# Performance work log

Measured on AMD Instinct MI355X. Metric: run time of the kernel, lower is better.

Reference implementation:

```python
import jax, jax.numpy as jnp
import numpy as np

LN_EPS = 1e-5

def silu(x):
    return x * jax.nn.sigmoid(x)

def setup_inputs() -> dict:
    key = jax.random.key(0)
    ks = jax.random.split(key, 24)
    B, D = 131072, 256
    def w(k, shape, fan_in):
        return jax.random.uniform(k, shape, jnp.float32, -1.0, 1.0) / np.sqrt(fan_in)
    inp = {
        'x': jax.random.normal(ks[0], (B, D), jnp.float32),
        # stem: Linear(D,128) -> LN(128) -> SiLU -> Linear(128,64) -> SiLU
        'stem_w1': w(ks[1], (D, 128), D), 'stem_b1': w(ks[2], (128,), D),
        'ln_g': jnp.ones((128,), jnp.float32), 'ln_b': jnp.zeros((128,), jnp.float32),
        'stem_w2': w(ks[3], (128, 64), 128), 'stem_b2': w(ks[4], (64,), 128),
        # 4 experts: Linear(64,128)->SiLU->Linear(128,64)->SiLU, stacked on axis 0
        'ew1': w(ks[5], (4, 64, 128), 64), 'eb1': w(ks[6], (4, 128), 64),
        'ew2': w(ks[7], (4, 128, 64), 128), 'eb2': w(ks[8], (4, 64), 128),
        # gate: Linear(64,32)->SiLU->Linear(32,4)
        'gw1': w(ks[9], (64, 32), 64), 'gb1': w(ks[10], (32,), 64),
        'gw2': w(ks[11], (32, 4), 32), 'gb2': w(ks[12], (4,), 32),
        # shared: Linear(64,64)->SiLU
        'sw': w(ks[13], (64, 64), 64), 'sb': w(ks[14], (64,), 64),
        # 3 heads (strain, tensile, yield) stacked: Linear(64,32)->SiLU->Linear(32,1)
        'hw1': w(ks[15], (3, 64, 32), 64), 'hb1': w(ks[16], (3, 32), 64),
        'hw2': w(ks[17], (3, 32, 1), 32), 'hb2': w(ks[18], (3, 1), 32),
    }
    return inp

def reference(x, stem_w1, stem_b1, ln_g, ln_b, stem_w2, stem_b2,
              ew1, eb1, ew2, eb2, gw1, gb1, gw2, gb2, sw, sb,
              hw1, hb1, hw2, hb2):
    # stem (dropout = identity, eval mode)
    h = x @ stem_w1 + stem_b1                      # [B,128]
    mu = jnp.mean(h, -1, keepdims=True)
    var = jnp.mean(jnp.square(h - mu), -1, keepdims=True)
    h = (h - mu) * jax.lax.rsqrt(var + LN_EPS) * ln_g + ln_b
    h = silu(h)
    h = silu(h @ stem_w2 + stem_b2)                # [B,64]
    # gate
    g = silu(h @ gw1 + gb1)
    gate_w = jax.nn.softmax(g @ gw2 + gb2, axis=-1)  # [B,4]
    # experts: [B,64] x [4,64,128] -> [B,4,128]
    e = silu(jnp.einsum('bd,edh->beh', h, ew1) + eb1)
    e = silu(jnp.einsum('beh,ehd->bed', e, ew2) + eb2)  # [B,4,64]
    moe_h = jnp.einsum('bed,be->bd', e, gate_w)    # [B,64]
    # shared trunk (dropout = identity)
    feat = silu(moe_h @ sw + sb)                   # [B,64]
    # 3 heads
    hh = silu(jnp.einsum('bd,kdh->bkh', feat, hw1) + hb1)  # [B,3,32]
    out = (jnp.einsum('bkh,kho->bko', hh, hw2) + hb2)[..., 0]  # [B,3]
    return out
```

## Files before the change

### kernel.cpp

```cpp
#include <hip/hip_runtime.h>

typedef _Float16 f16;
typedef f16   f16x4 __attribute__((ext_vector_type(4)));
typedef f16   f16x8 __attribute__((ext_vector_type(8)));
typedef float f32x4 __attribute__((ext_vector_type(4)));
typedef __attribute__((address_space(3))) char as3char;

#define MFMA16(a, b, c) __builtin_amdgcn_mfma_f32_16x16x32_f16((a), (b), (c), 0, 0, 0)

#define IMG_W1   0
#define IMG_W2   32768
#define IMG_GW1  40960
#define IMG_E    43008
#define IMG_SWH  108544
#define IMG_HW2G 116736

__device__ __forceinline__ float silu_f(float v) {
    return v * __builtin_amdgcn_rcpf(1.0f + __expf(-v));
}

__device__ void conv_blk(const float* __restrict__ src, f16* __restrict__ dst,
                         int srcN, int k0, int n0, int KB, int NB, int tid, int nth) {
    for (int i = tid; i < KB * NB; i += nth) {
        const int kk = i / NB, nn = i - kk * NB;
        dst[nn * KB + (kk ^ ((nn & 7) << 3))] = (f16)src[(long)(k0 + kk) * srcN + n0 + nn];
    }
}

__global__ void prep_weights(const float* __restrict__ w1, const float* __restrict__ w2,
                             const float* __restrict__ gw1, const float* __restrict__ ew1,
                             const float* __restrict__ ew2, const float* __restrict__ sw,
                             const float* __restrict__ hw1, f16* __restrict__ ws) {
    const int tid = blockIdx.x * 256 + threadIdx.x;
    const int nth = gridDim.x * 256;
    for (int kq = 0; kq < 4; ++kq)
        for (int nh = 0; nh < 2; ++nh)
            conv_blk(w1, ws + IMG_W1 + (kq * 2 + nh) * 4096, 128, kq * 64, nh * 64, 64, 64, tid, nth);
    for (int kh = 0; kh < 2; ++kh)
        conv_blk(w2, ws + IMG_W2 + kh * 4096, 64, kh * 64, 0, 64, 64, tid, nth);
    conv_blk(gw1, ws + IMG_GW1, 32, 0, 0, 64, 32, tid, nth);
    for (int e = 0; e < 4; ++e)
        for (int h = 0; h < 2; ++h) {
            conv_blk(ew1 + e * 8192, ws + IMG_E + e * 16384 + h * 8192,        128, 0, h * 64, 64, 64, tid, nth);
            conv_blk(ew2 + e * 8192, ws + IMG_E + e * 16384 + h * 8192 + 4096,  64, h * 64, 0, 64, 64, tid, nth);
        }
    conv_blk(sw, ws + IMG_SWH, 64, 0, 0, 64, 64, tid, nth);
    for (int h = 0; h < 2; ++h)
        conv_blk(hw1 + h * 2048, ws + IMG_SWH + 4096 + h * 2048, 32, 0, 0, 64, 32, tid, nth);
    conv_blk(hw1 + 2 * 2048, ws + IMG_HW2G, 32, 0, 0, 64, 32, tid, nth);
}

template<int BYTES>
__device__ __forceinline__ void stage4(const f16* __restrict__ g, as3char* l, int wv, int lane) {
    constexpr int CH = BYTES / 1024;
    #pragma unroll
    for (int ch = 0; ch < CH; ++ch)
        if ((ch & 3) == wv)
            __builtin_amdgcn_global_load_lds(
                (const __attribute__((address_space(1))) void*)((const char*)g + ch * 1024 + lane * 16),
                (__attribute__((address_space(3))) void*)(l + ch * 1024), 16, 0, 0);
}

__device__ __forceinline__ int swzW(int n) { return (n & 7) << 3; }
__device__ __forceinline__ int swzS(int r) { return (((((r >> 2) & 3) << 1) | (r & 1))) << 3; }

__device__ __forceinline__ f16x8 ldW(const f16* base, int row_base, int k0, int lane) {
    const int r = row_base + (lane & 15);
    const int k = k0 + ((lane >> 4) << 3);
    return *(const f16x8*)(base + r * 64 + (k ^ swzW(r)));
}
__device__ __forceinline__ f16x8 ldS(const f16* strip, int k0, int lane) {
    const int r = lane & 15;
    const int k = k0 + ((lane >> 4) << 3);
    return *(const f16x8*)(strip + r * 64 + (k ^ swzS(r)));
}
__device__ __forceinline__ void stS(f16* strip, int col_base, f32x4 v, int lane) {
    const int cc = col_base + (lane & 15);
    #pragma unroll
    for (int g = 0; g < 4; ++g) {
        const int r = ((lane >> 4) << 2) + g;
        strip[r * 64 + (cc ^ swzS(r))] = (f16)v[g];
    }
}

__device__ __forceinline__ void mm8(const f16x8 a[2], const f16* wb, f32x4 acc[4], int lane) {
    #pragma unroll
    for (int ks = 0; ks < 2; ++ks)
        #pragma unroll
        for (int n = 0; n < 4; ++n) {
            const f16x8 b = ldW(wb, n * 16, ks * 32, lane);
            acc[n] = MFMA16(a[ks], b, acc[n]);
        }
}

__device__ __forceinline__ void silu_to_frags(f16* strip, const f32x4 in[4], f16x8 outf[2], int lane) {
    #pragma unroll
    for (int n = 0; n < 4; ++n) {
        f32x4 v;
        #pragma unroll
        for (int g = 0; g < 4; ++g) v[g] = silu_f(in[n][g]);
        stS(strip, n * 16, v, lane);
    }
    #pragma unroll
    for (int ks = 0; ks < 2; ++ks)
        outf[ks] = ldS(strip, ks * 32, lane);
}

__device__ __forceinline__ f32x4 reduce16(f32x4 v) {
    #pragma unroll
    for (int m = 1; m <= 8; m <<= 1) {
        f32x4 o;
        #pragma unroll
        for (int i = 0; i < 4; ++i) o[i] = __shfl_xor(v[i], m, 64);
        v += o;
    }
    return v;
}

__global__ __launch_bounds__(256, 5)
void fused_net_mfma(const float* __restrict__ x,   const f16* __restrict__ wsp,
                    const float* __restrict__ b1,  const float* __restrict__ lng,
                    const float* __restrict__ lnb, const float* __restrict__ b2,
                    const float* __restrict__ eb1, const float* __restrict__ eb2,
                    const float* __restrict__ gb1, const float* __restrict__ gw2,
                    const float* __restrict__ gb2, const float* __restrict__ sb,
                    const float* __restrict__ hb1, const float* __restrict__ hw2,
                    const float* __restrict__ hb2, float* __restrict__ out)
{
    __shared__ __align__(16) f16 lds[14592];
    as3char* const LB = (as3char*)lds;
    const int lane = threadIdx.x & 63;
    const int wv   = threadIdx.x >> 6;
    const int c    = lane & 15;
    const int q    = lane >> 4;
    f16* STRIP = lds + wv * 1024;
    f16* const WB0 = lds + 4096;   as3char* const WB_3 = LB + 8192;
    f16* const WB1 = lds + 8192;
    f16* const G   = lds + 12288;  as3char* const G_3  = LB + 24576;
    f16* const GWT = lds + 14336;

    const long blockRow = (long)blockIdx.x * 64;
    const float* xw = x + (blockRow + wv * 16) * 256;

    stage4<16384>(wsp + IMG_W1, WB_3, wv, lane);
    stage4<4096>(wsp + IMG_GW1, G_3, wv, lane);
    __syncthreads();

    f32x4 acc[8];
    #pragma unroll
    for (int n8 = 0; n8 < 8; ++n8) {
        const float bv = b1[n8 * 16 + c];
        f32x4 t = {bv, bv, bv, bv};
        acc[n8] = t;
    }

    #pragma unroll 1
    for (int kq = 0; kq < 4; ++kq) {
        #pragma unroll
        for (int i = 0; i < 4; ++i) {
            const int idx4 = lane + i * 64;
            const int r  = idx4 >> 4;
            const int c4 = (idx4 & 15) << 2;
            const float4 v = *(const float4*)(xw + r * 256 + kq * 64 + c4);
            f16x4 o; o[0] = (f16)v.x; o[1] = (f16)v.y; o[2] = (f16)v.z; o[3] = (f16)v.w;
            *(f16x4*)(STRIP + r * 64 + (c4 ^ swzS(r))) = o;
        }
        f16x8 af[2];
        #pragma unroll
        for (int ks = 0; ks < 2; ++ks)
            af[ks] = ldS(STRIP, ks * 32, lane);

        mm8(af, WB0, acc,     lane);
        mm8(af, WB1, acc + 4, lane);
        __syncthreads();
        const f16* nsrc = (kq < 3) ? (wsp + IMG_W1 + (kq + 1) * 8192) : (wsp + IMG_W2);
        stage4<16384>(nsrc, WB_3, wv, lane);
        __syncthreads();
    }

    f32x4 mu, rs;
    {
        f32x4 s = {0,0,0,0}, qq = {0,0,0,0};
        #pragma unroll
        for (int n8 = 0; n8 < 8; ++n8) { s += acc[n8]; qq += acc[n8] * acc[n8]; }
        s = reduce16(s); qq = reduce16(qq);
        mu = s * 0.0078125f;
        #pragma unroll
        for (int g = 0; g < 4; ++g)
            rs[g] = rsqrtf(qq[g] * 0.0078125f - mu[g] * mu[g] + 1e-5f);
    }

    f32x4 a2[4];
    #pragma unroll
    for (int n = 0; n < 4; ++n) {
        const float bv = b2[n * 16 + c];
        f32x4 t = {bv, bv, bv, bv};
        a2[n] = t;
    }
    #pragma unroll
    for (int kh = 0; kh < 2; ++kh) {
        #pragma unroll
        for (int n = 0; n < 4; ++n) {
            const int j = kh * 64 + n * 16 + c;
            const float gg = lng[j], bb = lnb[j];
            f32x4 v;
            #pragma unroll
            for (int g = 0; g < 4; ++g)
                v[g] = silu_f((acc[kh * 4 + n][g] - mu[g]) * rs[g] * gg + bb);
            stS(STRIP, n * 16, v, lane);
        }
        f16x8 af[2];
        #pragma unroll
        for (int ks = 0; ks < 2; ++ks)
            af[ks] = ldS(STRIP, ks * 32, lane);
        mm8(af, kh == 0 ? WB0 : WB1, a2, lane);
    }
    f16x8 hbA[2];
    silu_to_frags(STRIP, a2, hbA, lane);

    {
        f32x4 ag[2];
        #pragma unroll
        for (int n = 0; n < 2; ++n) {
            const float bv = gb1[n * 16 + c];
            f32x4 t = {bv, bv, bv, bv};
            ag[n] = t;
        }
        #pragma unroll
        for (int ks = 0; ks < 2; ++ks)
            #pragma unroll
            for (int n = 0; n < 2; ++n) {
                const f16x8 b = ldW(G, n * 16, ks * 32, lane);
                ag[n] = MFMA16(hbA[ks], b, ag[n]);
            }
        const f32x4 gb2v = *(const f32x4*)gb2;
        f32x4 pg[4] = {{0,0,0,0},{0,0,0,0},{0,0,0,0},{0,0,0,0}};
        #pragma unroll
        for (int n = 0; n < 2; ++n) {
            const f32x4 w4 = *(const f32x4*)(gw2 + (n * 16 + c) * 4);
            #pragma unroll
            for (int g = 0; g < 4; ++g)
                pg[g] += silu_f(ag[n][g]) * w4;
        }
        #pragma unroll
        for (int g = 0; g < 4; ++g) {
            f32x4 l = reduce16(pg[g]) + gb2v;
            const float mx = fmaxf(fmaxf(l[0], l[1]), fmaxf(l[2], l[3]));
            f32x4 ee;
            #pragma unroll
            for (int o = 0; o < 4; ++o) ee[o] = __expf(l[o] - mx);
            const f32x4 gv = ee * __builtin_amdgcn_rcpf(ee[0] + ee[1] + ee[2] + ee[3]);
            if (c < 4) {
                const float val = (c == 0) ? gv[0] : (c == 1) ? gv[1] : (c == 2) ? gv[2] : gv[3];
                GWT[wv * 64 + c * 16 + q * 4 + g] = (f16)val;
            }
        }
    }

    f32x4 moe[4] = {{0,0,0,0},{0,0,0,0},{0,0,0,0},{0,0,0,0}};
    #pragma unroll 1
    for (int e = 0; e < 4; ++e) {
        f32x4 a2e[4];
        #pragma unroll
        for (int n = 0; n < 4; ++n) {
            const float bv = eb2[e * 64 + n * 16 + c];
            f32x4 t = {bv, bv, bv, bv};
            a2e[n] = t;
        }
        #pragma unroll
        for (int h = 0; h < 2; ++h) {
            __syncthreads();
            stage4<16384>(wsp + IMG_E + e * 16384 + h * 8192, WB_3, wv, lane);
            __syncthreads();
            f32x4 aa[4];
            #pragma unroll
            for (int n = 0; n < 4; ++n) {
                const float bv = eb1[e * 128 + h * 64 + n * 16 + c];
                f32x4 t = {bv, bv, bv, bv};
                aa[n] = t;
            }
            mm8(hbA, WB0, aa, lane);
            f16x8 ea[2];
            silu_to_frags(STRIP, aa, ea, lane);
            mm8(ea, WB1, a2e, lane);
        }
        #pragma unroll
        for (int g = 0; g < 4; ++g) {
            const float ge = (float)GWT[wv * 64 + e * 16 + q * 4 + g];
            #pragma unroll
            for (int n = 0; n < 4; ++n)
                moe[n][g] += silu_f(a2e[n][g]) * ge;
        }
    }

    __syncthreads();
    stage4<16384>(wsp + IMG_SWH, WB_3, wv, lane);
    stage4<4096>(wsp + IMG_HW2G, G_3, wv, lane);
    __syncthreads();

    f16x8 featA[2];
    {
        #pragma unroll
        for (int n = 0; n < 4; ++n)
            stS(STRIP, n * 16, moe[n], lane);
        f16x8 ma[2];
        #pragma unroll
        for (int ks = 0; ks < 2; ++ks)
            ma[ks] = ldS(STRIP, ks * 32, lane);
        f32x4 fs[4];
        #pragma unroll
        for (int n = 0; n < 4; ++n) {
            const float bv = sb[n * 16 + c];
            f32x4 t = {bv, bv, bv, bv};
            fs[n] = t;
        }
        mm8(ma, WB0, fs, lane);
        silu_to_frags(STRIP, fs, featA, lane);
    }

    {
        f32x4 ah[6];
        #pragma unroll
        for (int n = 0; n < 6; ++n) {
            const float bv = hb1[(n >> 1) * 32 + (n & 1) * 16 + c];
            f32x4 t = {bv, bv, bv, bv};
            ah[n] = t;
        }
        #pragma unroll
        for (int ks = 0; ks < 2; ++ks)
            #pragma unroll
            for (int n = 0; n < 6; ++n) {
                const int h = n >> 1;
                const f16* hw = (h == 0) ? WB1 : (h == 1) ? (WB1 + 2048) : G;
                const f16x8 b = ldW(hw, (n & 1) * 16, ks * 32, lane);
                ah[n] = MFMA16(featA[ks], b, ah[n]);
            }
        const float hb2_0 = hb2[0], hb2_1 = hb2[1], hb2_2 = hb2[2];
        f32x4 ph[3] = {{0,0,0,0},{0,0,0,0},{0,0,0,0}};
        #pragma unroll
        for (int n = 0; n < 6; ++n) {
            const int h = n >> 1;
            const float w2v = hw2[h * 32 + (n & 1) * 16 + c];
            #pragma unroll
            for (int g = 0; g < 4; ++g)
                ph[h][g] += silu_f(ah[n][g]) * w2v;
        }
        #pragma unroll
        for (int h = 0; h < 3; ++h) ph[h] = reduce16(ph[h]);
        #pragma unroll
        for (int g = 0; g < 4; ++g) {
            const long row = blockRow + wv * 16 + q * 4 + g;
            if (c < 3) {
                const float r0 = ph[0][g] + hb2_0;
                const float r1 = ph[1][g] + hb2_1;
                const float r2 = ph[2][g] + hb2_2;
                out[row * 3 + c] = (c == 0) ? r0 : ((c == 1) ? r1 : r2);
            }
        }
    }
}

extern "C" void kernel_launch(void* const* d_in, const int* in_sizes, int n_in,
                              void* d_out, int out_size, void* d_ws, size_t ws_size,
                              hipStream_t stream) {
    const float* x    = (const float*)d_in[0];
    const float* w1   = (const float*)d_in[1];
    const float* b1   = (const float*)d_in[2];
    const float* lng  = (const float*)d_in[3];
    const float* lnb  = (const float*)d_in[4];
    const float* w2   = (const float*)d_in[5];
    const float* b2   = (const float*)d_in[6];
    const float* ew1  = (const float*)d_in[7];
    const float* eb1  = (const float*)d_in[8];
    const float* ew2  = (const float*)d_in[9];
    const float* eb2  = (const float*)d_in[10];
    const float* gw1  = (const float*)d_in[11];
    const float* gb1  = (const float*)d_in[12];
    const float* gw2  = (const float*)d_in[13];
    const float* gb2  = (const float*)d_in[14];
    const float* sw   = (const float*)d_in[15];
    const float* sb   = (const float*)d_in[16];
    const float* hw1  = (const float*)d_in[17];
    const float* hb1  = (const float*)d_in[18];
    const float* hw2  = (const float*)d_in[19];
    const float* hb2  = (const float*)d_in[20];
    float* out = (float*)d_out;
    f16* ws = (f16*)d_ws;

    hipLaunchKernelGGL(prep_weights, dim3(64), dim3(256), 0, stream,
                       w1, w2, gw1, ew1, ew2, sw, hw1, ws);

    const int B = in_sizes[0] / 256;
    const int grid = B / 64;
    hipLaunchKernelGGL(fused_net_mfma, dim3(grid), dim3(256), 0, stream,
                       x, ws, b1, lng, lnb, b2, eb1, eb2, gb1, gw2, gb2,
                       sb, hb1, hw2, hb2, out);
}
```

Before: 104.2 us.

## Read MFMA weight fragments directly from global memory instead of LDS staging

Removes all global_load_lds staging of weight blocks into shared memory, along with the barriers around each stage. MFMA B fragments are now loaded straight from the pre-converted fp16 weight image in global memory, relying on L1/L2 caching. LDS shrinks to the per-wave strips plus the gate buffer, and launch bounds rise from 5 to 6 blocks per CU to use the freed occupancy. The risk is higher global and L2 traffic and latency per MFMA operand, since each wave now fetches weights separately instead of sharing one staged copy.

```diff
diff --git a/kernel.cpp b/kernel.cpp
--- a/kernel.cpp
+++ b/kernel.cpp
@@ -4,7 +4,6 @@
 typedef f16   f16x4 __attribute__((ext_vector_type(4)));
 typedef f16   f16x8 __attribute__((ext_vector_type(8)));
 typedef float f32x4 __attribute__((ext_vector_type(4)));
-typedef __attribute__((address_space(3))) char as3char;
 
 #define MFMA16(a, b, c) __builtin_amdgcn_mfma_f32_16x16x32_f16((a), (b), (c), 0, 0, 0)
 
@@ -50,21 +49,10 @@
     conv_blk(hw1 + 2 * 2048, ws + IMG_HW2G, 32, 0, 0, 64, 32, tid, nth);
 }
 
-template<int BYTES>
-__device__ __forceinline__ void stage4(const f16* __restrict__ g, as3char* l, int wv, int lane) {
-    constexpr int CH = BYTES / 1024;
-    #pragma unroll
-    for (int ch = 0; ch < CH; ++ch)
-        if ((ch & 3) == wv)
-            __builtin_amdgcn_global_load_lds(
-                (const __attribute__((address_space(1))) void*)((const char*)g + ch * 1024 + lane * 16),
-                (__attribute__((address_space(3))) void*)(l + ch * 1024), 16, 0, 0);
-}
-
 __device__ __forceinline__ int swzW(int n) { return (n & 7) << 3; }
 __device__ __forceinline__ int swzS(int r) { return (((((r >> 2) & 3) << 1) | (r & 1))) << 3; }
 
-__device__ __forceinline__ f16x8 ldW(const f16* base, int row_base, int k0, int lane) {
+__device__ __forceinline__ f16x8 ldW(const f16* __restrict__ base, int row_base, int k0, int lane) {
     const int r = row_base + (lane & 15);
     const int k = k0 + ((lane >> 4) << 3);
     return *(const f16x8*)(base + r * 64 + (k ^ swzW(r)));
@@ -83,7 +71,7 @@
     }
 }
 
-__device__ __forceinline__ void mm8(const f16x8 a[2], const f16* wb, f32x4 acc[4], int lane) {
+__device__ __forceinline__ void mm8(const f16x8 a[2], const f16* __restrict__ wb, f32x4 acc[4], int lane) {
     #pragma unroll
     for (int ks = 0; ks < 2; ++ks)
         #pragma unroll
@@ -117,7 +105,7 @@
     return v;
 }
 
-__global__ __launch_bounds__(256, 5)
+__global__ __launch_bounds__(256, 6)
 void fused_net_mfma(const float* __restrict__ x,   const f16* __restrict__ wsp,
                     const float* __restrict__ b1,  const float* __restrict__ lng,
                     const float* __restrict__ lnb, const float* __restrict__ b2,
@@ -127,24 +115,16 @@
                     const float* __restrict__ hb1, const float* __restrict__ hw2,
                     const float* __restrict__ hb2, float* __restrict__ out)
 {
-    __shared__ __align__(16) f16 lds[14592];
-    as3char* const LB = (as3char*)lds;
+    __shared__ __align__(16) f16 lds[4352];
     const int lane = threadIdx.x & 63;
     const int wv   = threadIdx.x >> 6;
     const int c    = lane & 15;
     const int q    = lane >> 4;
     f16* STRIP = lds + wv * 1024;
-    f16* const WB0 = lds + 4096;   as3char* const WB_3 = LB + 8192;
-    f16* const WB1 = lds + 8192;
-    f16* const G   = lds + 12288;  as3char* const G_3  = LB + 24576;
-    f16* const GWT = lds + 14336;
+    f16* const GWT = lds + 4096;
 
     const long blockRow = (long)blockIdx.x * 64;
     const float* xw = x + (blockRow + wv * 16) * 256;
-
-    stage4<16384>(wsp + IMG_W1, WB_3, wv, lane);
-    stage4<4096>(wsp + IMG_GW1, G_3, wv, lane);
-    __syncthreads();
 
     f32x4 acc[8];
     #pragma unroll
@@ -170,12 +150,8 @@
         for (int ks = 0; ks < 2; ++ks)
             af[ks] = ldS(STRIP, ks * 32, lane);
 
-        mm8(af, WB0, acc,     lane);
-        mm8(af, WB1, acc + 4, lane);
-        __syncthreads();
-        const f16* nsrc = (kq < 3) ? (wsp + IMG_W1 + (kq + 1) * 8192) : (wsp + IMG_W2);
-        stage4<16384>(nsrc, WB_3, wv, lane);
-        __syncthreads();
+        mm8(af, wsp + IMG_W1 + kq * 8192,        acc,     lane);
+        mm8(af, wsp + IMG_W1 + kq * 8192 + 4096, acc + 4, lane);
     }
 
     f32x4 mu, rs;
@@ -213,7 +189,7 @@
         #pragma unroll
         for (int ks = 0; ks < 2; ++ks)
             af[ks] = ldS(STRIP, ks * 32, lane);
-        mm8(af, kh == 0 ? WB0 : WB1, a2, lane);
+        mm8(af, wsp + IMG_W2 + kh * 4096, a2, lane);
     }
     f16x8 hbA[2];
     silu_to_frags(STRIP, a2, hbA, lane);
@@ -230,7 +206,7 @@
         for (int ks = 0; ks < 2; ++ks)
             #pragma unroll
             for (int n = 0; n < 2; ++n) {
-                const f16x8 b = ldW(G, n * 16, ks * 32, lane);
+                const f16x8 b = ldW(wsp + IMG_GW1, n * 16, ks * 32, lane);
                 ag[n] = MFMA16(hbA[ks], b, ag[n]);
             }
         const f32x4 gb2v = *(const f32x4*)gb2;
@@ -269,9 +245,7 @@
         }
         #pragma unroll
         for (int h = 0; h < 2; ++h) {
-            __syncthreads();
-            stage4<16384>(wsp + IMG_E + e * 16384 + h * 8192, WB_3, wv, lane);
-            __syncthreads();
+            const f16* ebase = wsp + IMG_E + e * 16384 + h * 8192;
             f32x4 aa[4];
             #pragma unroll
             for (int n = 0; n < 4; ++n) {
@@ -279,10 +253,10 @@
                 f32x4 t = {bv, bv, bv, bv};
                 aa[n] = t;
             }
-            mm8(hbA, WB0, aa, lane);
+            mm8(hbA, ebase, aa, lane);
             f16x8 ea[2];
             silu_to_frags(STRIP, aa, ea, lane);
-            mm8(ea, WB1, a2e, lane);
+            mm8(ea, ebase + 4096, a2e, lane);
         }
         #pragma unroll
         for (int g = 0; g < 4; ++g) {
@@ -292,11 +266,6 @@
                 moe[n][g] += silu_f(a2e[n][g]) * ge;
         }
     }
-
-    __syncthreads();
-    stage4<16384>(wsp + IMG_SWH, WB_3, wv, lane);
-    stage4<4096>(wsp + IMG_HW2G, G_3, wv, lane);
-    __syncthreads();
 
     f16x8 featA[2];
     {
@@ -314,7 +283,7 @@
             f32x4 t = {bv, bv, bv, bv};
             fs[n] = t;
         }
-        mm8(ma, WB0, fs, lane);
+        mm8(ma, wsp + IMG_SWH, fs, lane);
         silu_to_frags(STRIP, fs, featA, lane);
     }
 
@@ -331,7 +300,9 @@
             #pragma unroll
             for (int n = 0; n < 6; ++n) {
                 const int h = n >> 1;
-                const f16* hw = (h == 0) ? WB1 : (h == 1) ? (WB1 + 2048) : G;
+                const f16* hw = (h == 0) ? (wsp + IMG_SWH + 4096)
+                              : (h == 1) ? (wsp + IMG_SWH + 6144)
+                                         : (wsp + IMG_HW2G);
                 const f16x8 b = ldW(hw, (n & 1) * 16, ks * 32, lane);
                 ah[n] = MFMA16(featA[ks], b, ah[n]);
             }
```

Result: slower. 198.6 us (+90.7%).

## Process 32 rows per wave so each weight fragment feeds two MFMAs

Applied to the files above, without the earlier changes.

Each wave now handles two 16-row tiles (128 rows per block), and every B-fragment loaded from LDS is reused for two MFMAs. The weight staging buffer doubles to 32 KB, so fewer stage/sync rounds are needed, for example one round per expert instead of two. The aim is to halve LDS weight traffic and barrier overhead per row. In exchange the kernel holds twice the accumulators, lowers the launch_bounds occupancy target from 5 to 3, and runs half as many blocks, which reduces the latency hiding available.

```diff
diff --git a/kernel.cpp b/kernel.cpp
--- a/kernel.cpp
+++ b/kernel.cpp
@@ -13,7 +13,6 @@
 #define IMG_GW1  40960
 #define IMG_E    43008
 #define IMG_SWH  108544
-#define IMG_HW2G 116736
 
 __device__ __forceinline__ float silu_f(float v) {
     return v * __builtin_amdgcn_rcpf(1.0f + __expf(-v));
@@ -45,9 +44,8 @@
             conv_blk(ew2 + e * 8192, ws + IMG_E + e * 16384 + h * 8192 + 4096,  64, h * 64, 0, 64, 64, tid, nth);
         }
     conv_blk(sw, ws + IMG_SWH, 64, 0, 0, 64, 64, tid, nth);
-    for (int h = 0; h < 2; ++h)
+    for (int h = 0; h < 3; ++h)
         conv_blk(hw1 + h * 2048, ws + IMG_SWH + 4096 + h * 2048, 32, 0, 0, 64, 32, tid, nth);
-    conv_blk(hw1 + 2 * 2048, ws + IMG_HW2G, 32, 0, 0, 64, 32, tid, nth);
 }
 
 template<int BYTES>
@@ -69,41 +67,44 @@
     const int k = k0 + ((lane >> 4) << 3);
     return *(const f16x8*)(base + r * 64 + (k ^ swzW(r)));
 }
-__device__ __forceinline__ f16x8 ldS(const f16* strip, int k0, int lane) {
-    const int r = lane & 15;
+__device__ __forceinline__ f16x8 ldS(const f16* strip, int row_base, int k0, int lane) {
+    const int r = row_base + (lane & 15);
     const int k = k0 + ((lane >> 4) << 3);
     return *(const f16x8*)(strip + r * 64 + (k ^ swzS(r)));
 }
-__device__ __forceinline__ void stS(f16* strip, int col_base, f32x4 v, int lane) {
+__device__ __forceinline__ void stS(f16* strip, int row_base, int col_base, f32x4 v, int lane) {
     const int cc = col_base + (lane & 15);
     #pragma unroll
     for (int g = 0; g < 4; ++g) {
-        const int r = ((lane >> 4) << 2) + g;
+        const int r = row_base + ((lane >> 4) << 2) + g;
         strip[r * 64 + (cc ^ swzS(r))] = (f16)v[g];
     }
 }
 
-__device__ __forceinline__ void mm8(const f16x8 a[2], const f16* wb, f32x4 acc[4], int lane) {
+__device__ __forceinline__ void mm16(const f16x8 a0[2], const f16x8 a1[2],
+                                     const f16* wb, f32x4* c0, f32x4* c1, int lane) {
     #pragma unroll
     for (int ks = 0; ks < 2; ++ks)
         #pragma unroll
         for (int n = 0; n < 4; ++n) {
             const f16x8 b = ldW(wb, n * 16, ks * 32, lane);
-            acc[n] = MFMA16(a[ks], b, acc[n]);
-        }
-}
-
-__device__ __forceinline__ void silu_to_frags(f16* strip, const f32x4 in[4], f16x8 outf[2], int lane) {
+            c0[n] = MFMA16(a0[ks], b, c0[n]);
+            c1[n] = MFMA16(a1[ks], b, c1[n]);
+        }
+}
+
+__device__ __forceinline__ void silu_to_frags(f16* strip, int row_base, const f32x4 in[4],
+                                              f16x8 outf[2], int lane) {
     #pragma unroll
     for (int n = 0; n < 4; ++n) {
         f32x4 v;
         #pragma unroll
         for (int g = 0; g < 4; ++g) v[g] = silu_f(in[n][g]);
-        stS(strip, n * 16, v, lane);
+        stS(strip, row_base, n * 16, v, lane);
     }
     #pragma unroll
     for (int ks = 0; ks < 2; ++ks)
-        outf[ks] = ldS(strip, ks * 32, lane);
+        outf[ks] = ldS(strip, row_base, ks * 32, lane);
 }
 
 __device__ __forceinline__ f32x4 reduce16(f32x4 v) {
@@ -117,7 +118,7 @@
     return v;
 }
 
-__global__ __launch_bounds__(256, 5)
+__global__ __launch_bounds__(256, 3)
 void fused_net_mfma(const float* __restrict__ x,   const f16* __restrict__ wsp,
                     const float* __restrict__ b1,  const float* __restrict__ lng,
                     const float* __restrict__ lnb, const float* __restrict__ b2,
@@ -127,75 +128,89 @@
                     const float* __restrict__ hb1, const float* __restrict__ hw2,
                     const float* __restrict__ hb2, float* __restrict__ out)
 {
-    __shared__ __align__(16) f16 lds[14592];
+    __shared__ __align__(16) f16 lds[27136];
     as3char* const LB = (as3char*)lds;
     const int lane = threadIdx.x & 63;
     const int wv   = threadIdx.x >> 6;
     const int c    = lane & 15;
     const int q    = lane >> 4;
-    f16* STRIP = lds + wv * 1024;
-    f16* const WB0 = lds + 4096;   as3char* const WB_3 = LB + 8192;
-    f16* const WB1 = lds + 8192;
-    f16* const G   = lds + 12288;  as3char* const G_3  = LB + 24576;
-    f16* const GWT = lds + 14336;
-
-    const long blockRow = (long)blockIdx.x * 64;
-    const float* xw = x + (blockRow + wv * 16) * 256;
-
-    stage4<16384>(wsp + IMG_W1, WB_3, wv, lane);
+    f16* STRIP = lds + wv * 2048;
+    f16* const WB  = lds + 8192;   as3char* const WB_3 = LB + 16384;
+    f16* const G   = lds + 24576;  as3char* const G_3  = LB + 49152;
+    f16* const GWT = lds + 26624;
+
+    const long blockRow = (long)blockIdx.x * 128;
+    const float* xw = x + (blockRow + wv * 32) * 256;
+
+    stage4<32768>(wsp + IMG_W1, WB_3, wv, lane);
     stage4<4096>(wsp + IMG_GW1, G_3, wv, lane);
     __syncthreads();
 
-    f32x4 acc[8];
+    f32x4 acc0[8], acc1[8];
     #pragma unroll
     for (int n8 = 0; n8 < 8; ++n8) {
         const float bv = b1[n8 * 16 + c];
         f32x4 t = {bv, bv, bv, bv};
-        acc[n8] = t;
+        acc0[n8] = t; acc1[n8] = t;
     }
 
     #pragma unroll 1
-    for (int kq = 0; kq < 4; ++kq) {
-        #pragma unroll
-        for (int i = 0; i < 4; ++i) {
-            const int idx4 = lane + i * 64;
-            const int r  = idx4 >> 4;
-            const int c4 = (idx4 & 15) << 2;
-            const float4 v = *(const float4*)(xw + r * 256 + kq * 64 + c4);
-            f16x4 o; o[0] = (f16)v.x; o[1] = (f16)v.y; o[2] = (f16)v.z; o[3] = (f16)v.w;
-            *(f16x4*)(STRIP + r * 64 + (c4 ^ swzS(r))) = o;
-        }
-        f16x8 af[2];
-        #pragma unroll
-        for (int ks = 0; ks < 2; ++ks)
-            af[ks] = ldS(STRIP, ks * 32, lane);
-
-        mm8(af, WB0, acc,     lane);
-        mm8(af, WB1, acc + 4, lane);
+    for (int half = 0; half < 2; ++half) {
+        #pragma unroll
+        for (int j = 0; j < 2; ++j) {
+            const int kq = half * 2 + j;
+            #pragma unroll
+            for (int i = 0; i < 8; ++i) {
+                const int idx4 = lane + i * 64;
+                const int r  = idx4 >> 4;
+                const int c4 = (idx4 & 15) << 2;
+                const float4 v = *(const float4*)(xw + r * 256 + kq * 64 + c4);
+                f16x4 o; o[0] = (f16)v.x; o[1] = (f16)v.y; o[2] = (f16)v.z; o[3] = (f16)v.w;
+                *(f16x4*)(STRIP + r * 64 + (c4 ^ swzS(r))) = o;
+            }
+            f16x8 af0[2], af1[2];
+            #pragma unroll
+            for (int ks = 0; ks < 2; ++ks) {
+                af0[ks] = ldS(STRIP, 0,  ks * 32, lane);
+                af1[ks] = ldS(STRIP, 16, ks * 32, lane);
+            }
+            mm16(af0, af1, WB + (j * 2) * 4096,     acc0,     acc1,     lane);
+            mm16(af0, af1, WB + (j * 2 + 1) * 4096, acc0 + 4, acc1 + 4, lane);
+        }
         __syncthreads();
-        const f16* nsrc = (kq < 3) ? (wsp + IMG_W1 + (kq + 1) * 8192) : (wsp + IMG_W2);
-        stage4<16384>(nsrc, WB_3, wv, lane);
+        if (half == 0) stage4<32768>(wsp + IMG_W1 + 16384, WB_3, wv, lane);
+        else           stage4<16384>(wsp + IMG_W2,         WB_3, wv, lane);
         __syncthreads();
     }
 
-    f32x4 mu, rs;
+    f32x4 mu0, rs0, mu1, rs1;
     {
         f32x4 s = {0,0,0,0}, qq = {0,0,0,0};
         #pragma unroll
-        for (int n8 = 0; n8 < 8; ++n8) { s += acc[n8]; qq += acc[n8] * acc[n8]; }
+        for (int n8 = 0; n8 < 8; ++n8) { s += acc0[n8]; qq += acc0[n8] * acc0[n8]; }
         s = reduce16(s); qq = reduce16(qq);
-        mu = s * 0.0078125f;
+        mu0 = s * 0.0078125f;
         #pragma unroll
         for (int g = 0; g < 4; ++g)
-            rs[g] = rsqrtf(qq[g] * 0.0078125f - mu[g] * mu[g] + 1e-5f);
-    }
-
-    f32x4 a2[4];
+            rs0[g] = rsqrtf(qq[g] * 0.0078125f - mu0[g] * mu0[g] + 1e-5f);
+    }
+    {
+        f32x4 s = {0,0,0,0}, qq = {0,0,0,0};
+        #pragma unroll
+        for (int n8 = 0; n8 < 8; ++n8) { s += acc1[n8]; qq += acc1[n8] * acc1[n8]; }
+        s = reduce16(s); qq = reduce16(qq);
+        mu1 = s * 0.0078125f;
+        #pragma unroll
+        for (int g = 0; g < 4; ++g)
+            rs1[g] = rsqrtf(qq[g] * 0.0078125f - mu1[g] * mu1[g] + 1e-5f);
+    }
+
+    f32x4 a20[4], a21[4];
     #pragma unroll
     for (int n = 0; n < 4; ++n) {
         const float bv = b2[n * 16 + c];
         f32x4 t = {bv, bv, bv, bv};
-        a2[n] = t;
+        a20[n] = t; a21[n] = t;
     }
     #pragma unroll
     for (int kh = 0; kh < 2; ++kh) {
@@ -203,158 +218,182 @@
         for (int n = 0; n < 4; ++n) {
             const int j = kh * 64 + n * 16 + c;
             const float gg = lng[j], bb = lnb[j];
-            f32x4 v;
-            #pragma unroll
-            for (int g = 0; g < 4; ++g)
-                v[g] = silu_f((acc[kh * 4 + n][g] - mu[g]) * rs[g] * gg + bb);
-            stS(STRIP, n * 16, v, lane);
-        }
-        f16x8 af[2];
-        #pragma unroll
-        for (int ks = 0; ks < 2; ++ks)
-            af[ks] = ldS(STRIP, ks * 32, lane);
-        mm8(af, kh == 0 ? WB0 : WB1, a2, lane);
-    }
-    f16x8 hbA[2];
-    silu_to_frags(STRIP, a2, hbA, lane);
+            f32x4 v0, v1;
+            #pragma unroll
+            for (int g = 0; g < 4; ++g) {
+                v0[g] = silu_f((acc0[kh * 4 + n][g] - mu0[g]) * rs0[g] * gg + bb);
+                v1[g] = silu_f((acc1[kh * 4 + n][g] - mu1[g]) * rs1[g] * gg + bb);
+            }
+            stS(STRIP, 0,  n * 16, v0, lane);
+            stS(STRIP, 16, n * 16, v1, lane);
+        }
+        f16x8 af0[2], af1[2];
+        #pragma unroll
+        for (int ks = 0; ks < 2; ++ks) {
+            af0[ks] = ldS(STRIP, 0,  ks * 32, lane);
+            af1[ks] = ldS(STRIP, 16, ks * 32, lane);
+        }
+        mm16(af0, af1, WB + kh * 4096, a20, a21, lane);
+    }
+    f16x8 hbA0[2], hbA1[2];
+    silu_to_frags(STRIP, 0,  a20, hbA0, lane);
+    silu_to_frags(STRIP, 16, a21, hbA1, lane);
 
     {
-        f32x4 ag[2];
+        f32x4 ag0[2], ag1[2];
         #pragma unroll
         for (int n = 0; n < 2; ++n) {
             const float bv = gb1[n * 16 + c];
             f32x4 t = {bv, bv, bv, bv};
-            ag[n] = t;
+            ag0[n] = t; ag1[n] = t;
         }
         #pragma unroll
         for (int ks = 0; ks < 2; ++ks)
             #pragma unroll
             for (int n = 0; n < 2; ++n) {
                 const f16x8 b = ldW(G, n * 16, ks * 32, lane);
-                ag[n] = MFMA16(hbA[ks], b, ag[n]);
+                ag0[n] = MFMA16(hbA0[ks], b, ag0[n]);
+                ag1[n] = MFMA16(hbA1[ks], b, ag1[n]);
             }
         const f32x4 gb2v = *(const f32x4*)gb2;
-        f32x4 pg[4] = {{0,0,0,0},{0,0,0,0},{0,0,0,0},{0,0,0,0}};
-        #pragma unroll
-        for (int n = 0; n < 2; ++n) {
-            const f32x4 w4 = *(const f32x4*)(gw2 + (n * 16 + c) * 4);
-            #pragma unroll
-            for (int g = 0; g < 4; ++g)
-                pg[g] += silu_f(ag[n][g]) * w4;
-        }
-        #pragma unroll
-        for (int g = 0; g < 4; ++g) {
-            f32x4 l = reduce16(pg[g]) + gb2v;
-            const float mx = fmaxf(fmaxf(l[0], l[1]), fmaxf(l[2], l[3]));
-            f32x4 ee;
-            #pragma unroll
-            for (int o = 0; o < 4; ++o) ee[o] = __expf(l[o] - mx);
-            const f32x4 gv = ee * __builtin_amdgcn_rcpf(ee[0] + ee[1] + ee[2] + ee[3]);
-            if (c < 4) {
-                const float val = (c == 0) ? gv[0] : (c == 1) ? gv[1] : (c == 2) ? gv[2] : gv[3];
-                GWT[wv * 64 + c * 16 + q * 4 + g] = (f16)val;
-            }
-        }
-    }
-
-    f32x4 moe[4] = {{0,0,0,0},{0,0,0,0},{0,0,0,0},{0,0,0,0}};
+        #pragma unroll
+        for (int m = 0; m < 2; ++m) {
+            f32x4 pg[4] = {{0,0,0,0},{0,0,0,0},{0,0,0,0},{0,0,0,0}};
+            #pragma unroll
+            for (int n = 0; n < 2; ++n) {
+                const f32x4 w4 = *(const f32x4*)(gw2 + (n * 16 + c) * 4);
+                #pragma unroll
+                for (int g = 0; g < 4; ++g)
+                    pg[g] += silu_f(m == 0 ? ag0[n][g] : ag1[n][g]) * w4;
+            }
+            #pragma unroll
+            for (int g = 0; g < 4; ++g) {
+                f32x4 l = reduce16(pg[g]) + gb2v;
+                const float mx = fmaxf(fmaxf(l[0], l[1]), fmaxf(l[2], l[3]));
+                f32x4 ee;
+                #pragma unroll
+                for (int o = 0; o < 4; ++o) ee[o] = __expf(l[o] - mx);
+                const f32x4 gv = ee * __builtin_amdgcn_rcpf(ee[0] + ee[1] + ee[2] + ee[3]);
+                if (c < 4) {
+                    const float val = (c == 0) ? gv[0] : (c == 1) ? gv[1] : (c == 2) ? gv[2] : gv[3];
+                    GWT[wv * 128 + c * 32 + m * 16 + q * 4 + g] = (f16)val;
+                }
+            }
+        }
+    }
+    __syncthreads();
+    stage4<32768>(wsp + IMG_E, WB_3, wv, lane);
+    __syncthreads();
+
+    f32x4 moe0[4] = {{0,0,0,0},{0,0,0,0},{0,0,0,0},{0,0,0,0}};
+    f32x4 moe1[4] = {{0,0,0,0},{0,0,0,0},{0,0,0,0},{0,0,0,0}};
     #pragma unroll 1
     for (int e = 0; e < 4; ++e) {
-        f32x4 a2e[4];
+        f32x4 a2e0[4], a2e1[4];
         #pragma unroll
         for (int n = 0; n < 4; ++n) {
             const float bv = eb2[e * 64 + n * 16 + c];
             f32x4 t = {bv, bv, bv, bv};
-            a2e[n] = t;
+            a2e0[n] = t; a2e1[n] = t;
         }
         #pragma unroll
         for (int h = 0; h < 2; ++h) {
-            __syncthreads();
-            stage4<16384>(wsp + IMG_E + e * 16384 + h * 8192, WB_3, wv, lane);
-            __syncthreads();
-            f32x4 aa[4];
+            const f16* ebase = WB + h * 8192;
+            f32x4 aa0[4], aa1[4];
             #pragma unroll
             for (int n = 0; n < 4; ++n) {
                 const float bv = eb1[e * 128 + h * 64 + n * 16 + c];
                 f32x4 t = {bv, bv, bv, bv};
-                aa[n] = t;
-            }
-            mm8(hbA, WB0, aa, lane);
-            f16x8 ea[2];
-            silu_to_frags(STRIP, aa, ea, lane);
-            mm8(ea, WB1, a2e, lane);
-        }
-        #pragma unroll
-        for (int g = 0; g < 4; ++g) {
-            const float ge = (float)GWT[wv * 64 + e * 16 + q * 4 + g];
-            #pragma unroll
-            for (int n = 0; n < 4; ++n)
-                moe[n][g] += silu_f(a2e[n][g]) * ge;
-        }
-    }
-
-    __syncthreads();
-    stage4<16384>(wsp + IMG_SWH, WB_3, wv, lane);
-    stage4<4096>(wsp + IMG_HW2G, G_3, wv, lane);
-    __syncthreads();
-
-    f16x8 featA[2];
+                aa0[n] = t; aa1[n] = t;
+            }
+            mm16(hbA0, hbA1, ebase, aa0, aa1, lane);
+            f16x8 ea0[2], ea1[2];
+            silu_to_frags(STRIP, 0,  aa0, ea0, lane);
+            silu_to_frags(STRIP, 16, aa1, ea1, lane);
+            mm16(ea0, ea1, ebase + 4096, a2e0, a2e1, lane);
+        }
+        #pragma unroll
+        for (int m = 0; m < 2; ++m)
+            #pragma unroll
+            for (int g = 0; g < 4; ++g) {
+                const float ge = (float)GWT[wv * 128 + e * 32 + m * 16 + q * 4 + g];
+                #pragma unroll
+                for (int n = 0; n < 4; ++n) {
+                    if (m == 0) moe0[n][g] += silu_f(a2e0[n][g]) * ge;
+                    else        moe1[n][g] += silu_f(a2e1[n][g]) * ge;
+                }
+            }
+        __syncthreads();
+        if (e < 3) stage4<32768>(wsp + IMG_E + (e + 1) * 16384, WB_3, wv, lane);
+        else       stage4<20480>(wsp + IMG_SWH, WB_3, wv, lane);
+        __syncthreads();
+    }
+
+    f16x8 featA0[2], featA1[2];
     {
         #pragma unroll
-        for (int n = 0; n < 4; ++n)
-            stS(STRIP, n * 16, moe[n], lane);
-        f16x8 ma[2];
-        #pragma unroll
-        for (int ks = 0; ks < 2; ++ks)
-            ma[ks] = ldS(STRIP, ks * 32, lane);
-        f32x4 fs[4];
+        for (int n = 0; n < 4; ++n) {
+            stS(STRIP, 0,  n * 16, moe0[n], lane);
+            stS(STRIP, 16, n * 16, moe1[n], lane);
+        }
+        f16x8 ma0[2], ma1[2];
+        #pragma unroll
+        for (int ks = 0; ks < 2; ++ks) {
+            ma0[ks] = ldS(STRIP, 0,  ks * 32, lane);
+            ma1[ks] = ldS(STRIP, 16, ks * 32, lane);
+        }
+        f32x4 fs0[4], fs1[4];
         #pragma unroll
         for (int n = 0; n < 4; ++n) {
             const float bv = sb[n * 16 + c];
             f32x4 t = {bv, bv, bv, bv};
-            fs[n] = t;
-        }
-        mm8(ma, WB0, fs, lane);
-        silu_to_frags(STRIP, fs, featA, lane);
+            fs0[n] = t; fs1[n] = t;
+        }
+        mm16(ma0, ma1, WB, fs0, fs1, lane);
+        silu_to_frags(STRIP, 0,  fs0, featA0, lane);
+        silu_to_frags(STRIP, 16, fs1, featA1, lane);
     }
 
     {
-        f32x4 ah[6];
+        f32x4 ah0[6], ah1[6];
         #pragma unroll
         for (int n = 0; n < 6; ++n) {
             const float bv = hb1[(n >> 1) * 32 + (n & 1) * 16 + c];
             f32x4 t = {bv, bv, bv, bv};
-            ah[n] = t;
+            ah0[n] = t; ah1[n] = t;
         }
         #pragma unroll
         for (int ks = 0; ks < 2; ++ks)
+            #pragma unroll
+            for (int n = 0; n < 6; ++n) {
+                const f16* hw = WB + 4096 + (n >> 1) * 2048;
+                const f16x8 b = ldW(hw, (n & 1) * 16, ks * 32, lane);
+                ah0[n] = MFMA16(featA0[ks], b, ah0[n]);
+                ah1[n] = MFMA16(featA1[ks], b, ah1[n]);
+            }
+        const float hb2_0 = hb2[0], hb2_1 = hb2[1], hb2_2 = hb2[2];
+        #pragma unroll
+        for (int m = 0; m < 2; ++m) {
+            f32x4 ph[3] = {{0,0,0,0},{0,0,0,0},{0,0,0,0}};
             #pragma unroll
             for (int n = 0; n < 6; ++n) {
                 const int h = n >> 1;
-                const f16* hw = (h == 0) ? WB1 : (h == 1) ? (WB1 + 2048) : G;
-                const f16x8 b = ldW(hw, (n & 1) * 16, ks * 32, lane);
-                ah[n] = MFMA16(featA[ks], b, ah[n]);
-            }
-        const float hb2_0 = hb2[0], hb2_1 = hb2[1], hb2_2 = hb2[2];
-        f32x4 ph[3] = {{0,0,0,0},{0,0,0,0},{0,0,0,0}};
-        #pragma unroll
-        for (int n = 0; n < 6; ++n) {
-            const int h = n >> 1;
-            const float w2v = hw2[h * 32 + (n & 1) * 16 + c];
-            #pragma unroll
-            for (int g = 0; g < 4; ++g)
-                ph[h][g] += silu_f(ah[n][g]) * w2v;
-        }
-        #pragma unroll
-        for (int h = 0; h < 3; ++h) ph[h] = reduce16(ph[h]);
-        #pragma unroll
-        for (int g = 0; g < 4; ++g) {
-            const long row = blockRow + wv * 16 + q * 4 + g;
-            if (c < 3) {
-                const float r0 = ph[0][g] + hb2_0;
-                const float r1 = ph[1][g] + hb2_1;
-                const float r2 = ph[2][g] + hb2_2;
-                out[row * 3 + c] = (c == 0) ? r0 : ((c == 1) ? r1 : r2);
+                const float w2v = hw2[h * 32 + (n & 1) * 16 + c];
+                #pragma unroll
+                for (int g = 0; g < 4; ++g)
+                    ph[h][g] += silu_f(m == 0 ? ah0[n][g] : ah1[n][g]) * w2v;
+            }
+            #pragma unroll
+            for (int h = 0; h < 3; ++h) ph[h] = reduce16(ph[h]);
+            #pragma unroll
+            for (int g = 0; g < 4; ++g) {
+                const long row = blockRow + wv * 32 + m * 16 + q * 4 + g;
+                if (c < 3) {
+                    const float r0 = ph[0][g] + hb2_0;
+                    const float r1 = ph[1][g] + hb2_1;
+                    const float r2 = ph[2][g] + hb2_2;
+                    out[row * 3 + c] = (c == 0) ? r0 : ((c == 1) ? r1 : r2);
+                }
             }
         }
     }
@@ -391,7 +430,7 @@
                        w1, w2, gw1, ew1, ew2, sw, hw1, ws);
 
     const int B = in_sizes[0] / 256;
-    const int grid = B / 64;
+    const int grid = B / 128;
     hipLaunchKernelGGL(fused_net_mfma, dim3(grid), dim3(256), 0, stream,
                        x, ws, b1, lng, lnb, b2, eb1, eb2, gb1, gw2, gb2,
                        sb, hb1, hw2, hb2, out);
```

Measured after the change: 142.3 us. 1.37x slower.

## Double-buffer weight stages in LDS and register-prefetch input tiles

Applied to the files above, without the earlier changes.

Splits the weight area of LDS into two buffers (WA/WB). Each next weight chunk (stem W1 slices, W2, expert halves, shared and head weights) is loaded asynchronously into one buffer while MFMA runs on the other, which removes most of the stage-then-sync stalls. Input x slices are also prefetched into registers one k-step ahead. The head weights are repacked into one contiguous image so they can be staged together. The cost is a much larger LDS footprint, with launch bounds lowered from 5 to 4 blocks, so occupancy drops.

```diff
diff --git a/kernel.cpp b/kernel.cpp
--- a/kernel.cpp
+++ b/kernel.cpp
@@ -13,7 +13,6 @@
 #define IMG_GW1  40960
 #define IMG_E    43008
 #define IMG_SWH  108544
-#define IMG_HW2G 116736
 
 __device__ __forceinline__ float silu_f(float v) {
     return v * __builtin_amdgcn_rcpf(1.0f + __expf(-v));
@@ -45,9 +44,8 @@
             conv_blk(ew2 + e * 8192, ws + IMG_E + e * 16384 + h * 8192 + 4096,  64, h * 64, 0, 64, 64, tid, nth);
         }
     conv_blk(sw, ws + IMG_SWH, 64, 0, 0, 64, 64, tid, nth);
-    for (int h = 0; h < 2; ++h)
+    for (int h = 0; h < 3; ++h)
         conv_blk(hw1 + h * 2048, ws + IMG_SWH + 4096 + h * 2048, 32, 0, 0, 64, 32, tid, nth);
-    conv_blk(hw1 + 2 * 2048, ws + IMG_HW2G, 32, 0, 0, 64, 32, tid, nth);
 }
 
 template<int BYTES>
@@ -117,7 +115,7 @@
     return v;
 }
 
-__global__ __launch_bounds__(256, 5)
+__global__ __launch_bounds__(256, 4)
 void fused_net_mfma(const float* __restrict__ x,   const f16* __restrict__ wsp,
                     const float* __restrict__ b1,  const float* __restrict__ lng,
                     const float* __restrict__ lnb, const float* __restrict__ b2,
@@ -127,23 +125,29 @@
                     const float* __restrict__ hb1, const float* __restrict__ hw2,
                     const float* __restrict__ hb2, float* __restrict__ out)
 {
-    __shared__ __align__(16) f16 lds[14592];
+    __shared__ __align__(16) f16 lds[22784];
     as3char* const LB = (as3char*)lds;
     const int lane = threadIdx.x & 63;
     const int wv   = threadIdx.x >> 6;
     const int c    = lane & 15;
     const int q    = lane >> 4;
     f16* STRIP = lds + wv * 1024;
-    f16* const WB0 = lds + 4096;   as3char* const WB_3 = LB + 8192;
-    f16* const WB1 = lds + 8192;
-    f16* const G   = lds + 12288;  as3char* const G_3  = LB + 24576;
-    f16* const GWT = lds + 14336;
+    f16* const WA = lds + 4096;   as3char* const WA_3 = LB + 8192;
+    f16* const WB = lds + 12288;  as3char* const WB_3 = LB + 24576;
+    f16* const G  = lds + 20480;  as3char* const G_3  = LB + 40960;
+    f16* const GWT = lds + 22528;
 
     const long blockRow = (long)blockIdx.x * 64;
     const float* xw = x + (blockRow + wv * 16) * 256;
 
-    stage4<16384>(wsp + IMG_W1, WB_3, wv, lane);
+    stage4<16384>(wsp + IMG_W1, WA_3, wv, lane);
     stage4<4096>(wsp + IMG_GW1, G_3, wv, lane);
+    float4 xr[4];
+    #pragma unroll
+    for (int i = 0; i < 4; ++i) {
+        const int idx4 = lane + i * 64;
+        xr[i] = *(const float4*)(xw + (idx4 >> 4) * 256 + ((idx4 & 15) << 2));
+    }
     __syncthreads();
 
     f32x4 acc[8];
@@ -154,27 +158,33 @@
         acc[n8] = t;
     }
 
-    #pragma unroll 1
+    #pragma unroll
     for (int kq = 0; kq < 4; ++kq) {
+        const f16* cur  = (kq & 1) ? WB : WA;
+        as3char* nxt3   = (kq & 1) ? WA_3 : WB_3;
+        if (kq < 3) stage4<16384>(wsp + IMG_W1 + (kq + 1) * 8192, nxt3, wv, lane);
+        else        stage4<16384>(wsp + IMG_W2, nxt3, wv, lane);
         #pragma unroll
         for (int i = 0; i < 4; ++i) {
             const int idx4 = lane + i * 64;
             const int r  = idx4 >> 4;
             const int c4 = (idx4 & 15) << 2;
-            const float4 v = *(const float4*)(xw + r * 256 + kq * 64 + c4);
-            f16x4 o; o[0] = (f16)v.x; o[1] = (f16)v.y; o[2] = (f16)v.z; o[3] = (f16)v.w;
+            f16x4 o; o[0] = (f16)xr[i].x; o[1] = (f16)xr[i].y; o[2] = (f16)xr[i].z; o[3] = (f16)xr[i].w;
             *(f16x4*)(STRIP + r * 64 + (c4 ^ swzS(r))) = o;
         }
         f16x8 af[2];
         #pragma unroll
         for (int ks = 0; ks < 2; ++ks)
             af[ks] = ldS(STRIP, ks * 32, lane);
-
-        mm8(af, WB0, acc,     lane);
-        mm8(af, WB1, acc + 4, lane);
-        __syncthreads();
-        const f16* nsrc = (kq < 3) ? (wsp + IMG_W1 + (kq + 1) * 8192) : (wsp + IMG_W2);
-        stage4<16384>(nsrc, WB_3, wv, lane);
+        if (kq < 3) {
+            #pragma unroll
+            for (int i = 0; i < 4; ++i) {
+                const int idx4 = lane + i * 64;
+                xr[i] = *(const float4*)(xw + (idx4 >> 4) * 256 + (kq + 1) * 64 + ((idx4 & 15) << 2));
+            }
+        }
+        mm8(af, cur,        acc,     lane);
+        mm8(af, cur + 4096, acc + 4, lane);
         __syncthreads();
     }
 
@@ -190,6 +200,7 @@
             rs[g] = rsqrtf(qq[g] * 0.0078125f - mu[g] * mu[g] + 1e-5f);
     }
 
+    stage4<16384>(wsp + IMG_E, WB_3, wv, lane);
     f32x4 a2[4];
     #pragma unroll
     for (int n = 0; n < 4; ++n) {
@@ -213,7 +224,7 @@
         #pragma unroll
         for (int ks = 0; ks < 2; ++ks)
             af[ks] = ldS(STRIP, ks * 32, lane);
-        mm8(af, kh == 0 ? WB0 : WB1, a2, lane);
+        mm8(af, WA + kh * 4096, a2, lane);
     }
     f16x8 hbA[2];
     silu_to_frags(STRIP, a2, hbA, lane);
@@ -256,6 +267,7 @@
             }
         }
     }
+    __syncthreads();
 
     f32x4 moe[4] = {{0,0,0,0},{0,0,0,0},{0,0,0,0},{0,0,0,0}};
     #pragma unroll 1
@@ -267,22 +279,35 @@
             f32x4 t = {bv, bv, bv, bv};
             a2e[n] = t;
         }
-        #pragma unroll
-        for (int h = 0; h < 2; ++h) {
-            __syncthreads();
-            stage4<16384>(wsp + IMG_E + e * 16384 + h * 8192, WB_3, wv, lane);
-            __syncthreads();
+        stage4<16384>(wsp + IMG_E + e * 16384 + 8192, WA_3, wv, lane);
+        {
             f32x4 aa[4];
             #pragma unroll
             for (int n = 0; n < 4; ++n) {
-                const float bv = eb1[e * 128 + h * 64 + n * 16 + c];
+                const float bv = eb1[e * 128 + n * 16 + c];
                 f32x4 t = {bv, bv, bv, bv};
                 aa[n] = t;
             }
-            mm8(hbA, WB0, aa, lane);
+            mm8(hbA, WB, aa, lane);
             f16x8 ea[2];
             silu_to_frags(STRIP, aa, ea, lane);
-            mm8(ea, WB1, a2e, lane);
+            mm8(ea, WB + 4096, a2e, lane);
+        }
+        __syncthreads();
+        if (e < 3) stage4<16384>(wsp + IMG_E + (e + 1) * 16384, WB_3, wv, lane);
+        else       stage4<12288>(wsp + IMG_SWH, WB_3, wv, lane);
+        {
+            f32x4 aa[4];
+            #pragma unroll
+            for (int n = 0; n < 4; ++n) {
+                const float bv = eb1[e * 128 + 64 + n * 16 + c];
+                f32x4 t = {bv, bv, bv, bv};
+                aa[n] = t;
+            }
+            mm8(hbA, WA, aa, lane);
+            f16x8 ea[2];
+            silu_to_frags(STRIP, aa, ea, lane);
+            mm8(ea, WA + 4096, a2e, lane);
         }
         #pragma unroll
         for (int g = 0; g < 4; ++g) {
@@ -291,13 +316,10 @@
             for (int n = 0; n < 4; ++n)
                 moe[n][g] += silu_f(a2e[n][g]) * ge;
         }
-    }
-
-    __syncthreads();
-    stage4<16384>(wsp + IMG_SWH, WB_3, wv, lane);
-    stage4<4096>(wsp + IMG_HW2G, G_3, wv, lane);
-    __syncthreads();
-
+        __syncthreads();
+    }
+
+    stage4<8192>(wsp + IMG_SWH + 6144, WA_3, wv, lane);
     f16x8 featA[2];
     {
         #pragma unroll
@@ -314,9 +336,10 @@
             f32x4 t = {bv, bv, bv, bv};
             fs[n] = t;
         }
-        mm8(ma, WB0, fs, lane);
+        mm8(ma, WB, fs, lane);
         silu_to_frags(STRIP, fs, featA, lane);
     }
+    __syncthreads();
 
     {
         f32x4 ah[6];
@@ -331,7 +354,7 @@
             #pragma unroll
             for (int n = 0; n < 6; ++n) {
                 const int h = n >> 1;
-                const f16* hw = (h == 0) ? WB1 : (h == 1) ? (WB1 + 2048) : G;
+                const f16* hw = (h == 0) ? (WB + 4096) : (h == 1) ? WA : (WA + 2048);
                 const f16x8 b = ldW(hw, (n & 1) * 16, ks * 32, lane);
                 ah[n] = MFMA16(featA[ks], b, ah[n]);
             }
```

After: 120.7 us. 15.8% more time.
